# Kernel optimization log

Hardware: AMD Instinct MI355X
Metric: run time of the kernel (lower is better)

## Reference

```python
import jax, jax.numpy as jnp
import numpy as np

B, S, F, H, P, O = 512, 336, 16, 256, 48, 1

def _gru_cell(x, h, Wih, Whh, bih, bhh):
    # torch GRU gate order: r, z, n
    gx = x @ Wih.T + bih            # [B, 3H]
    gh = h @ Whh.T + bhh            # [B, 3H]
    rx, zx, nx = jnp.split(gx, 3, axis=-1)
    rh, zh, nh = jnp.split(gh, 3, axis=-1)
    r = jax.nn.sigmoid(rx + rh)
    z = jax.nn.sigmoid(zx + zh)
    n = jnp.tanh(nx + r * nh)
    return (1.0 - z) * n + z * h

def setup_inputs() -> dict:
    key = jax.random.key(0)
    ks = jax.random.split(key, 12)
    s = lambda *sh: 1.0 / np.sqrt(sh[-1])
    d = {}
    d["xb"] = jax.random.normal(ks[0], (B, S, F), dtype=jnp.float32)
    # encoder GRU (1 layer, unidirectional)
    d["enc_Wih"] = jax.random.normal(ks[1], (3 * H, F), dtype=jnp.float32) * s(F)
    d["enc_Whh"] = jax.random.normal(ks[2], (3 * H, H), dtype=jnp.float32) * s(H)
    d["enc_bih"] = jnp.zeros((3 * H,), dtype=jnp.float32)
    d["enc_bhh"] = jnp.zeros((3 * H,), dtype=jnp.float32)
    # attention linear: (H + F) -> S
    d["att_W"] = jax.random.normal(ks[3], (S, H + F), dtype=jnp.float32) * s(H + F)
    d["att_b"] = jnp.zeros((S,), dtype=jnp.float32)
    # decoder GRUCell: input H, hidden H
    d["dec_Wih"] = jax.random.normal(ks[4], (3 * H, H), dtype=jnp.float32) * s(H)
    d["dec_Whh"] = jax.random.normal(ks[5], (3 * H, H), dtype=jnp.float32) * s(H)
    d["dec_bih"] = jnp.zeros((3 * H,), dtype=jnp.float32)
    d["dec_bhh"] = jnp.zeros((3 * H,), dtype=jnp.float32)
    # decoder output: H -> F
    d["out_W"] = jax.random.normal(ks[6], (F, H), dtype=jnp.float32) * s(H)
    d["out_b"] = jnp.zeros((F,), dtype=jnp.float32)
    # final linear: F -> O
    d["lin_W"] = jax.random.normal(ks[7], (O, F), dtype=jnp.float32) * s(F)
    d["lin_b"] = jnp.zeros((O,), dtype=jnp.float32)
    return d

def reference(xb, enc_Wih, enc_Whh, enc_bih, enc_bhh, att_W, att_b,
              dec_Wih, dec_Whh, dec_bih, dec_bhh, out_W, out_b, lin_W, lin_b):
    # ---- encoder: GRU over time ----
    h0 = jnp.zeros((B, H), dtype=xb.dtype)
    xs = jnp.swapaxes(xb, 0, 1)  # [S, B, F]

    def enc_step(h, x):
        h2 = _gru_cell(x, h, enc_Wih, enc_Whh, enc_bih, enc_bhh)
        return h2, h2

    enc_hidden, enc_out = jax.lax.scan(enc_step, h0, xs)
    enc_out = jnp.swapaxes(enc_out, 0, 1)  # [B, S, H]

    # ---- decoder: per-step attention + GRUCell + output proj ----
    y0 = xb[:, -1, :]  # [B, F]

    def dec_step(carry, _):
        h, y = carry
        att_in = jnp.concatenate([h, y], axis=1)          # [B, H+F]
        attn = jax.nn.softmax(att_in @ att_W.T + att_b, axis=-1)  # [B, S]
        combine = jnp.einsum('bs,bsh->bh', attn, enc_out)  # [B, H]
        h2 = _gru_cell(combine, h, dec_Wih, dec_Whh, dec_bih, dec_bhh)
        out = h2 @ out_W.T + out_b                         # [B, F]
        return (h2, out), out

    _, outs = jax.lax.scan(dec_step, (enc_hidden, y0), None, length=P)  # [P, B, F]
    outs = jnp.swapaxes(outs, 0, 1)                        # [B, P, F]
    outs = outs @ lin_W.T + lin_b                          # [B, P, O]
    return outs.squeeze(-1)                                # [B, P]
```

## Files before the change

### kernel.cpp

```cpp
#include <hip/hip_runtime.h>
#include <cstdint>
#include <cstddef>

#define B_ 512
#define S_ 336
#define F_ 16
#define H_ 256
#define P_ 48

typedef __bf16 bhalf;
typedef __attribute__((ext_vector_type(8))) __bf16 bhalf8;
typedef __attribute__((ext_vector_type(4))) float f32x4;

#define MFMA16(A, Bv, C) __builtin_amdgcn_mfma_f32_16x16x32_bf16((A), (Bv), (C), 0, 0, 0)

__device__ __forceinline__ float fastrcp(float x) { return __builtin_amdgcn_rcpf(x); }
__device__ __forceinline__ float sigm(float x) { return fastrcp(1.0f + __expf(-x)); }
__device__ __forceinline__ float tanh_f(float x) { return 2.0f * fastrcp(1.0f + __expf(-2.0f * x)) - 1.0f; }

__device__ __forceinline__ bhalf u16_to_bf(unsigned int u) {
  return __builtin_bit_cast(__bf16, (unsigned short)u);
}
__device__ __forceinline__ unsigned short bf_to_u16(bhalf b) {
  return __builtin_bit_cast(unsigned short, b);
}

__device__ __forceinline__ bhalf8 bzero8() {
  bhalf8 v;
#pragma unroll
  for (int j = 0; j < 8; ++j) v[j] = (bhalf)0.0f;
  return v;
}

__global__ __launch_bounds__(256, 1) void enc_kernel(
    const float* __restrict__ Whh, const float* __restrict__ Wih,
    const float* __restrict__ bih, const float* __restrict__ bhh,
    const float* __restrict__ xb,
    bhalf* __restrict__ enc_out,
    float* __restrict__ hcur,
    unsigned int* __restrict__ hpack,
    unsigned int* __restrict__ flags)
{
  const int tid  = threadIdx.x;
  const int lane = tid & 63;
  const int wv   = tid >> 6;
  const int ncol = lane & 15;
  const int quad = lane >> 4;

  const int blk = blockIdx.x;
  const int g   = blk & 31;
  const int w   = blk >> 5;
  const int b0  = g * 16;
  const int i0  = w * 64 + wv * 16;

  bhalf8 bWh[3][9], bWl[3][9];
#pragma unroll
  for (int gg = 0; gg < 3; ++gg) {
    const int jrow = gg * 256 + i0 + ncol;
#pragma unroll
    for (int kt = 0; kt < 9; ++kt) {
      bhalf8 vh = bzero8(), vl = bzero8();
      if (kt < 8) {
        const float* src = Whh + (size_t)jrow * 256 + kt * 32 + quad * 8;
#pragma unroll
        for (int j = 0; j < 8; ++j) {
          const float v = src[j];
          const bhalf h = (bhalf)v;
          vh[j] = h;
          vl[j] = (bhalf)(v - (float)h);
        }
      } else if (quad < 2) {
        const float* src = Wih + (size_t)jrow * 16 + quad * 8;
#pragma unroll
        for (int j = 0; j < 8; ++j) {
          const float v = src[j];
          const bhalf h = (bhalf)v;
          vh[j] = h;
          vl[j] = (bhalf)(v - (float)h);
        }
      }
      bWh[gg][kt] = vh;
      bWl[gg][kt] = vl;
    }
  }

  const int jr = i0 + ncol;
  const float bR  = bih[jr]       + bhh[jr];
  const float bZ  = bih[256 + jr] + bhh[256 + jr];
  const float bNx = bih[512 + jr];
  const float bNh = bhh[512 + jr];

  const int bA = b0 + ncol;
  const int kA = quad * 8;

  float hold[4] = {0.0f, 0.0f, 0.0f, 0.0f};

  for (int t = 0; t < S_; ++t) {
    bhalf8 xh = bzero8(), xl = bzero8();
    if (quad < 2) {
      const float* xp = xb + ((size_t)bA * S_ + t) * F_ + quad * 8;
#pragma unroll
      for (int j = 0; j < 8; ++j) {
        const float v = __builtin_nontemporal_load(xp + j);
        const bhalf h = (bhalf)v;
        xh[j] = h;
        xl[j] = (bhalf)(v - (float)h);
      }
    }

    f32x4 aR0 = {0,0,0,0}, aR1 = {0,0,0,0}, aR2 = {0,0,0,0};
    f32x4 aZ0 = {0,0,0,0}, aZ1 = {0,0,0,0}, aZ2 = {0,0,0,0};
    f32x4 aN0 = {0,0,0,0}, aN1 = {0,0,0,0}, aN2 = {0,0,0,0};
    f32x4 aNx = {0,0,0,0};

    aR0 = MFMA16(xh, bWh[0][8], aR0);
    aR1 = MFMA16(xh, bWl[0][8], aR1);
    aR2 = MFMA16(xl, bWh[0][8], aR2);
    aZ0 = MFMA16(xh, bWh[1][8], aZ0);
    aZ1 = MFMA16(xh, bWl[1][8], aZ1);
    aZ2 = MFMA16(xl, bWh[1][8], aZ2);
    aNx = MFMA16(xh, bWh[2][8], aNx);
    aNx = MFMA16(xh, bWl[2][8], aNx);
    aNx = MFMA16(xl, bWh[2][8], aNx);

    if (t > 0) {
      const unsigned int* fp = &flags[g * 4 + (lane & 3)];
      while (__hip_atomic_load(fp, __ATOMIC_RELAXED, __HIP_MEMORY_SCOPE_AGENT) <
             (unsigned int)t)
        __builtin_amdgcn_s_sleep(1);

      const int slot = (t - 1) & 1;
      const unsigned long long* hp64 =
          (const unsigned long long*)(hpack + ((size_t)slot * B_ + bA) * H_ + kA);

      unsigned long long wbuf[32];
#pragma unroll
      for (int i = 0; i < 32; ++i)
        wbuf[i] = __hip_atomic_load(hp64 + (i >> 2) * 16 + (i & 3),
                                    __ATOMIC_RELAXED, __HIP_MEMORY_SCOPE_AGENT);

#pragma unroll
      for (int kt = 0; kt < 8; ++kt) {
        bhalf8 Ah, Al;
#pragma unroll
        for (int j2 = 0; j2 < 4; ++j2) {
          const unsigned long long w2 = wbuf[kt * 4 + j2];
          Ah[2 * j2]     = u16_to_bf((unsigned int)w2);
          Al[2 * j2]     = u16_to_bf((unsigned int)(w2 >> 16));
          Ah[2 * j2 + 1] = u16_to_bf((unsigned int)(w2 >> 32));
          Al[2 * j2 + 1] = u16_to_bf((unsigned int)(w2 >> 48));
        }
        aR0 = MFMA16(Ah, bWh[0][kt], aR0);
        aR1 = MFMA16(Ah, bWl[0][kt], aR1);
        aR2 = MFMA16(Al, bWh[0][kt], aR2);
        aZ0 = MFMA16(Ah, bWh[1][kt], aZ0);
        aZ1 = MFMA16(Ah, bWl[1][kt], aZ1);
        aZ2 = MFMA16(Al, bWh[1][kt], aZ2);
        aN0 = MFMA16(Ah, bWh[2][kt], aN0);
        aN1 = MFMA16(Ah, bWl[2][kt], aN1);
        aN2 = MFMA16(Al, bWh[2][kt], aN2);
      }
    }

    const int iL = i0 + ncol;
    bhalf his[4];
#pragma unroll
    for (int r = 0; r < 4; ++r) {
      const float sR  = aR0[r] + aR1[r] + aR2[r] + bR;
      const float sZ  = aZ0[r] + aZ1[r] + aZ2[r] + bZ;
      const float nhv = aN0[r] + aN1[r] + aN2[r] + bNh;
      const float nxv = aNx[r] + bNx;
      const float rr = sigm(sR);
      const float zz = sigm(sZ);
      const float nn = tanh_f(nxv + rr * nhv);
      const float h2 = (1.0f - zz) * nn + zz * hold[r];
      hold[r] = h2;
      his[r] = (bhalf)h2;
      const bhalf lo = (bhalf)(h2 - (float)his[r]);
      const int bb = b0 + quad * 4 + r;
      const unsigned int wrd =
          (unsigned int)bf_to_u16(his[r]) | ((unsigned int)bf_to_u16(lo) << 16);
      __hip_atomic_store(&hpack[((size_t)(t & 1) * B_ + bb) * H_ + iL], wrd,
                         __ATOMIC_RELAXED, __HIP_MEMORY_SCOPE_AGENT);
    }

    __syncthreads();
    if (tid == 0) {
      __hip_atomic_store(&flags[g * 4 + w], (unsigned int)(t + 1),
                         __ATOMIC_RELAXED, __HIP_MEMORY_SCOPE_AGENT);
    }

#pragma unroll
    for (int r = 0; r < 4; ++r) {
      const int bb = b0 + quad * 4 + r;
      __builtin_nontemporal_store(his[r], enc_out + ((size_t)bb * S_ + t) * H_ + iL);
    }
  }

#pragma unroll
  for (int r = 0; r < 4; ++r)
    hcur[(size_t)(b0 + quad * 4 + r) * H_ + i0 + ncol] = hold[r];
}

__global__ __launch_bounds__(256) void wpack_kernel(const float* __restrict__ Whh,
                                                    const float* __restrict__ Wih,
                                                    bhalf* __restrict__ wbT) {
  const int idx = blockIdx.x * 256 + threadIdx.x;
  if (idx >= 64 * 768 * 8) return;
  const int j = idx & 7;
  const int row = (idx >> 3) % 768;
  const int k8 = idx / (768 * 8);
  const int k = k8 * 8 + j;
  const float v = (k < 256) ? Whh[(size_t)row * 256 + k]
                            : Wih[(size_t)row * 256 + (k - 256)];
  wbT[idx] = (bhalf)v;
}

__global__ __launch_bounds__(256) void apack_kernel(const float* __restrict__ attW,
                                                    bhalf* __restrict__ abT) {
  const int idx = blockIdx.x * 256 + threadIdx.x;
  if (idx >= 36 * 336 * 8) return;
  const int j = idx & 7;
  const int s = (idx >> 3) % 336;
  const int k8 = idx / (8 * 336);
  const int k = k8 * 8 + j;
  abT[idx] = (k < 272) ? (bhalf)attW[(size_t)s * 272 + k] : (bhalf)0.0f;
}

__global__ __launch_bounds__(256) void dec_kernel(
    const bhalf* __restrict__ wbT,
    const bhalf* __restrict__ abT,
    const float* __restrict__ attb,
    const float* __restrict__ bih, const float* __restrict__ bhh,
    const float* __restrict__ outW, const float* __restrict__ outb,
    const float* __restrict__ linW, const float* __restrict__ linb,
    const bhalf* __restrict__ enc_out, const float* __restrict__ hcur,
    const float* __restrict__ xb, float* __restrict__ dout)
{
  __shared__ __align__(16) bhalf encL[126 * 256];
  __shared__ __align__(16) float hybuf[2][288];
  __shared__ __align__(16) float cL[256];
  __shared__ float sc[S_];
  __shared__ float pC[8][32][9];
  __shared__ float red[8];
  const int tid  = threadIdx.x;
  const int lane = tid & 63;
  const int wv   = tid >> 6;
  const int b    = blockIdx.x;
  const int jj   = tid;
  const int cg   = tid & 31;
  const int ck   = tid >> 5;
  const int s2ok = tid < 80;
  const int f_o  = tid >> 4;
  const int q_o  = tid & 15;

  {
    const bhalf8* src = (const bhalf8*)(enc_out + (size_t)b * S_ * H_);
    bhalf8* dst = (bhalf8*)encL;
    for (int it = tid; it < 126 * 32; it += 256) dst[it] = src[it];
  }

  hybuf[0][tid] = hcur[(size_t)b * H_ + tid];
  if (tid < 16) {
    hybuf[0][256 + tid] = xb[((size_t)b * S_ + (S_ - 1)) * F_ + tid];
    hybuf[1][256 + tid] = 0.0f;
  } else if (tid < 32) {
    hybuf[0][256 + tid] = 0.0f;
    hybuf[1][256 + tid] = 0.0f;
  }

  const float bRv  = bih[jj]       + bhh[jj];
  const float bZv  = bih[256 + jj] + bhh[256 + jj];
  const float bNxv = bih[512 + jj];
  const float bNhv = bhh[512 + jj];

  const float ab1 = attb[tid];
  const float ab2 = s2ok ? attb[tid + 256] : 0.0f;

  f32x4 ow[4];
  {
    const float* wrp = outW + (size_t)f_o * H_ + q_o * 16;
#pragma unroll
    for (int jv = 0; jv < 4; ++jv) ow[jv] = *(const f32x4*)(wrp + jv * 4);
  }
  const float outb_f = outb[f_o];
  const float linw_t = (tid < 16) ? linW[tid] : 0.0f;
  const float linb0  = linb[0];

  const bhalf* epC = enc_out + ((size_t)b * S_ + ck * 42) * H_ + cg * 8;
  const bhalf* epL = encL + (size_t)(ck * 42) * H_ + cg * 8;
  __syncthreads();

  for (int p = 0; p < P_; ++p) {
    float* hc = hybuf[p & 1];
    float* hn = hybuf[(p & 1) ^ 1];

    float v1, v2 = -3.0e38f;
    {
      float d0 = 0, d1 = 0, d2 = 0, d3 = 0;
#pragma unroll 4
      for (int k8 = 0; k8 < 36; ++k8) {
        const bhalf8 q = *(const bhalf8*)(abT + ((size_t)k8 * S_ + tid) * 8);
        const float* v = hc + k8 * 8;
        d0 += (float)q[0] * v[0] + (float)q[4] * v[4];
        d1 += (float)q[1] * v[1] + (float)q[5] * v[5];
        d2 += (float)q[2] * v[2] + (float)q[6] * v[6];
        d3 += (float)q[3] * v[3] + (float)q[7] * v[7];
      }
      v1 = d0 + d1 + d2 + d3 + ab1;
    }
    if (s2ok) {
      float d0 = 0, d1 = 0, d2 = 0, d3 = 0;
#pragma unroll 4
      for (int k8 = 0; k8 < 36; ++k8) {
        const bhalf8 q = *(const bhalf8*)(abT + ((size_t)k8 * S_ + tid + 256) * 8);
        const float* v = hc + k8 * 8;
        d0 += (float)q[0] * v[0] + (float)q[4] * v[4];
        d1 += (float)q[1] * v[1] + (float)q[5] * v[5];
        d2 += (float)q[2] * v[2] + (float)q[6] * v[6];
        d3 += (float)q[3] * v[3] + (float)q[7] * v[7];
      }
      v2 = d0 + d1 + d2 + d3 + ab2;
    }

    float m = fmaxf(v1, v2);
#pragma unroll
    for (int o = 32; o > 0; o >>= 1) m = fmaxf(m, __shfl_xor(m, o, 64));
    if (lane == 0) red[wv] = m;
    __syncthreads();
    const float mx = fmaxf(fmaxf(red[0], red[1]), fmaxf(red[2], red[3]));
    const float e1 = __expf(v1 - mx);
    sc[tid] = e1;
    float e2 = 0.0f;
    if (s2ok) { e2 = __expf(v2 - mx); sc[tid + 256] = e2; }
    float sum = e1 + e2;
#pragma unroll
    for (int o = 32; o > 0; o >>= 1) sum += __shfl_xor(sum, o, 64);
    if (lane == 0) red[4 + wv] = sum;
    __syncthreads();
    const float inv = fastrcp(red[4] + red[5] + red[6] + red[7]);

    {
      float a0 = 0, a1 = 0, a2 = 0, a3 = 0, a4 = 0, a5 = 0, a6 = 0, a7 = 0;
      const float* scrow = sc + ck * 42;
      if (ck < 3) {
#pragma unroll 6
        for (int s5 = 0; s5 < 42; ++s5) {
          const bhalf8 v = *(const bhalf8*)(epL + (size_t)s5 * H_);
          const float wgt = scrow[s5];
          a0 += wgt * (float)v[0];
          a1 += wgt * (float)v[1];
          a2 += wgt * (float)v[2];
          a3 += wgt * (float)v[3];
          a4 += wgt * (float)v[4];
          a5 += wgt * (float)v[5];
          a6 += wgt * (float)v[6];
          a7 += wgt * (float)v[7];
        }
      } else {
#pragma unroll 6
        for (int s5 = 0; s5 < 42; ++s5) {
          const bhalf8 v = *(const bhalf8*)(epC + (size_t)s5 * H_);
          const float wgt = scrow[s5];
          a0 += wgt * (float)v[0];
          a1 += wgt * (float)v[1];
          a2 += wgt * (float)v[2];
          a3 += wgt * (float)v[3];
          a4 += wgt * (float)v[4];
          a5 += wgt * (float)v[5];
          a6 += wgt * (float)v[6];
          a7 += wgt * (float)v[7];
        }
      }
      float* pp = pC[ck][cg];
      pp[0] = a0; pp[1] = a1; pp[2] = a2; pp[3] = a3;
      pp[4] = a4; pp[5] = a5; pp[6] = a6; pp[7] = a7;
    }
    __syncthreads();

    float r0 = 0, r1 = 0, z0 = 0, z1 = 0, nh0 = 0, nh1 = 0, nx0 = 0, nx1 = 0;
    {
      const int gg = jj >> 3, j = jj & 7;
      float ssum = 0.0f;
#pragma unroll
      for (int c = 0; c < 8; ++c) ssum += pC[c][gg][j];
      cL[jj] = ssum * inv;
    }
#pragma unroll 4
    for (int k8 = 0; k8 < 32; ++k8) {
      const bhalf* base = wbT + ((size_t)k8 * 768) * 8;
      const bhalf8 qR = *(const bhalf8*)(base + (size_t)jj * 8);
      const bhalf8 qZ = *(const bhalf8*)(base + (size_t)(256 + jj) * 8);
      const bhalf8 qN = *(const bhalf8*)(base + (size_t)(512 + jj) * 8);
      const float* v = hc + k8 * 8;
      r0 += (float)qR[0]*v[0] + (float)qR[2]*v[2] + (float)qR[4]*v[4] + (float)qR[6]*v[6];
      r1 += (float)qR[1]*v[1] + (float)qR[3]*v[3] + (float)qR[5]*v[5] + (float)qR[7]*v[7];
      z0 += (float)qZ[0]*v[0] + (float)qZ[2]*v[2] + (float)qZ[4]*v[4] + (float)qZ[6]*v[6];
      z1 += (float)qZ[1]*v[1] + (float)qZ[3]*v[3] + (float)qZ[5]*v[5] + (float)qZ[7]*v[7];
      nh0 += (float)qN[0]*v[0] + (float)qN[2]*v[2] + (float)qN[4]*v[4] + (float)qN[6]*v[6];
      nh1 += (float)qN[1]*v[1] + (float)qN[3]*v[3] + (float)qN[5]*v[5] + (float)qN[7]*v[7];
    }
    __syncthreads();
#pragma unroll 4
    for (int k8 = 32; k8 < 64; ++k8) {
      const bhalf* base = wbT + ((size_t)k8 * 768) * 8;
      const bhalf8 qR = *(const bhalf8*)(base + (size_t)jj * 8);
      const bhalf8 qZ = *(const bhalf8*)(base + (size_t)(256 + jj) * 8);
      const bhalf8 qN = *(const bhalf8*)(base + (size_t)(512 + jj) * 8);
      const float* v = cL + (k8 - 32) * 8;
      r0 += (float)qR[0]*v[0] + (float)qR[2]*v[2] + (float)qR[4]*v[4] + (float)qR[6]*v[6];
      r1 += (float)qR[1]*v[1] + (float)qR[3]*v[3] + (float)qR[5]*v[5] + (float)qR[7]*v[7];
      z0 += (float)qZ[0]*v[0] + (float)qZ[2]*v[2] + (float)qZ[4]*v[4] + (float)qZ[6]*v[6];
      z1 += (float)qZ[1]*v[1] + (float)qZ[3]*v[3] + (float)qZ[5]*v[5] + (float)qZ[7]*v[7];
      nx0 += (float)qN[0]*v[0] + (float)qN[2]*v[2] + (float)qN[4]*v[4] + (float)qN[6]*v[6];
      nx1 += (float)qN[1]*v[1] + (float)qN[3]*v[3] + (float)qN[5]*v[5] + (float)qN[7]*v[7];
    }
    {
      const float sR = r0 + r1 + bRv;
      const float sZ = z0 + z1 + bZv;
      const float nh = nh0 + nh1 + bNhv;
      const float nx = nx0 + nx1 + bNxv;
      const float rr = 1.0f / (1.0f + __expf(-sR));
      const float zz = 1.0f / (1.0f + __expf(-sZ));
      const float nn = tanhf(nx + rr * nh);
      hn[jj] = (1.0f - zz) * nn + zz * hc[jj];
    }
    __syncthreads();

    {
      const float* hv = hn + q_o * 16;
      float a0 = 0, a1 = 0, a2 = 0, a3 = 0;
#pragma unroll
      for (int jv = 0; jv < 4; ++jv) {
        const f32x4 h4 = *(const f32x4*)(hv + jv * 4);
        a0 += ow[jv][0] * h4[0]; a1 += ow[jv][1] * h4[1];
        a2 += ow[jv][2] * h4[2]; a3 += ow[jv][3] * h4[3];
      }
      float a = a0 + a1 + a2 + a3;
      a += __shfl_xor(a, 1, 64); a += __shfl_xor(a, 2, 64);
      a += __shfl_xor(a, 4, 64); a += __shfl_xor(a, 8, 64);
      if (q_o == 0) hn[256 + f_o] = a + outb_f;
    }
    __syncthreads();
    if (tid < 16) {
      float v = hn[256 + tid] * linw_t;
      v += __shfl_xor(v, 1, 64); v += __shfl_xor(v, 2, 64);
      v += __shfl_xor(v, 4, 64); v += __shfl_xor(v, 8, 64);
      if (tid == 0) dout[(size_t)b * P_ + p] = v + linb0;
    }
  }
}

extern "C" void kernel_launch(void* const* d_in, const int* in_sizes, int n_in,
                              void* d_out, int out_size, void* d_ws, size_t ws_size,
                              hipStream_t stream)
{
  (void)in_sizes; (void)n_in; (void)out_size;
  const float* xb      = (const float*)d_in[0];
  const float* enc_Wih = (const float*)d_in[1];
  const float* enc_Whh = (const float*)d_in[2];
  const float* enc_bih = (const float*)d_in[3];
  const float* enc_bhh = (const float*)d_in[4];
  const float* att_W   = (const float*)d_in[5];
  const float* att_b   = (const float*)d_in[6];
  const float* dec_Wih = (const float*)d_in[7];
  const float* dec_Whh = (const float*)d_in[8];
  const float* dec_bih = (const float*)d_in[9];
  const float* dec_bhh = (const float*)d_in[10];
  const float* out_W   = (const float*)d_in[11];
  const float* out_b   = (const float*)d_in[12];
  const float* lin_W   = (const float*)d_in[13];
  const float* lin_b   = (const float*)d_in[14];
  float* dout = (float*)d_out;

  char* ws = (char*)d_ws;
  const size_t off_enc = 0;
  const size_t off_hp  = off_enc + (size_t)B_ * S_ * H_ * 2;
  const size_t off_hc  = off_hp + (size_t)2 * B_ * H_ * 4;
  const size_t off_wb  = off_hc + (size_t)B_ * H_ * 4;
  const size_t off_ab  = off_wb + (size_t)64 * 768 * 8 * 2;
  const size_t off_fl  = off_ab + (size_t)36 * 336 * 8 * 2;
  const size_t need    = off_fl + 32 * 8 * sizeof(unsigned int);
  if (ws_size < need) return;

  bhalf* enc_out      = (bhalf*)(ws + off_enc);
  unsigned int* hpack = (unsigned int*)(ws + off_hp);
  float* hcur         = (float*)(ws + off_hc);
  bhalf* wbT          = (bhalf*)(ws + off_wb);
  bhalf* abT          = (bhalf*)(ws + off_ab);
  unsigned int* flags = (unsigned int*)(ws + off_fl);

  (void)hipMemsetAsync(flags, 0, 32 * 8 * sizeof(unsigned int), stream);
  wpack_kernel<<<(64 * 768 * 8 + 255) / 256, 256, 0, stream>>>(dec_Whh, dec_Wih, wbT);
  apack_kernel<<<(36 * 336 * 8 + 255) / 256, 256, 0, stream>>>(att_W, abT);
  enc_kernel<<<128, 256, 0, stream>>>(enc_Whh, enc_Wih, enc_bih, enc_bhh, xb,
                                      enc_out, hcur, hpack, flags);
  dec_kernel<<<B_, 256, 0, stream>>>(wbT, abT, att_b, dec_bih, dec_bhh,
                                     out_W, out_b, lin_W, lin_b,
                                     enc_out, hcur, xb, dout);
}
```

Baseline: 3.254 ms.

## Replace cross-block flag-synchronized encoder with per-block LDS recurrence

The encoder GRU previously split each 16-row batch group across 4 blocks that exchanged hidden state through global memory with atomic flags and spin-waits every timestep. It now runs one 512-thread block per batch group, keeping the hi/lo bf16 hidden state in double-buffered shared memory and synchronizing with __syncthreads. Weights are pre-packed by a new kernel into an MFMA-fragment layout and streamed from global/L2 each step rather than held in registers. This removes the inter-block spin latency, but it uses only 32 blocks and re-reads about 860 KB of weights per step, which may make each step memory-bound.

```diff
diff --git a/kernel.cpp b/kernel.cpp
--- a/kernel.cpp
+++ b/kernel.cpp
@@ -18,13 +18,6 @@
 __device__ __forceinline__ float sigm(float x) { return fastrcp(1.0f + __expf(-x)); }
 __device__ __forceinline__ float tanh_f(float x) { return 2.0f * fastrcp(1.0f + __expf(-2.0f * x)) - 1.0f; }
 
-__device__ __forceinline__ bhalf u16_to_bf(unsigned int u) {
-  return __builtin_bit_cast(__bf16, (unsigned short)u);
-}
-__device__ __forceinline__ unsigned short bf_to_u16(bhalf b) {
-  return __builtin_bit_cast(unsigned short, b);
-}
-
 __device__ __forceinline__ bhalf8 bzero8() {
   bhalf8 v;
 #pragma unroll
@@ -32,70 +25,66 @@
   return v;
 }
 
-__global__ __launch_bounds__(256, 1) void enc_kernel(
-    const float* __restrict__ Whh, const float* __restrict__ Wih,
+__global__ __launch_bounds__(256) void epack_kernel(const float* __restrict__ Whh,
+                                                    const float* __restrict__ Wih,
+                                                    bhalf* __restrict__ epk) {
+  const int idx = blockIdx.x * 256 + threadIdx.x;
+  if (idx >= 2 * 48 * 9 * 64 * 8) return;
+  const int jj   = idx & 7;
+  const int lane = (idx >> 3) & 63;
+  const int kt   = (idx >> 9) % 9;
+  const int tile = (idx / (512 * 9)) % 48;
+  const int pl   = idx / (512 * 9 * 48);
+  const int wv = tile / 6, rem = tile % 6, gg = rem >> 1, q = rem & 1;
+  const int ncol = lane & 15, quad = lane >> 4;
+  const int jrow = gg * 256 + wv * 32 + q * 16 + ncol;
+  const int k = kt * 32 + quad * 8 + jj;
+  float v = 0.0f;
+  if (k < 256) v = Whh[(size_t)jrow * 256 + k];
+  else if (k < 272) v = Wih[(size_t)jrow * 16 + (k - 256)];
+  const bhalf hi = (bhalf)v;
+  epk[idx] = (pl == 0) ? hi : (bhalf)(v - (float)hi);
+}
+
+__global__ __launch_bounds__(512, 1) void enc2_kernel(
+    const bhalf* __restrict__ epk,
     const float* __restrict__ bih, const float* __restrict__ bhh,
     const float* __restrict__ xb,
     bhalf* __restrict__ enc_out,
-    float* __restrict__ hcur,
-    unsigned int* __restrict__ hpack,
-    unsigned int* __restrict__ flags)
+    float* __restrict__ hcur)
 {
+  __shared__ __align__(16) bhalf hb[2][2][16][264];
+
   const int tid  = threadIdx.x;
   const int lane = tid & 63;
   const int wv   = tid >> 6;
   const int ncol = lane & 15;
   const int quad = lane >> 4;
-
-  const int blk = blockIdx.x;
-  const int g   = blk & 31;
-  const int w   = blk >> 5;
-  const int b0  = g * 16;
-  const int i0  = w * 64 + wv * 16;
-
-  bhalf8 bWh[3][9], bWl[3][9];
-#pragma unroll
-  for (int gg = 0; gg < 3; ++gg) {
-    const int jrow = gg * 256 + i0 + ncol;
-#pragma unroll
-    for (int kt = 0; kt < 9; ++kt) {
-      bhalf8 vh = bzero8(), vl = bzero8();
-      if (kt < 8) {
-        const float* src = Whh + (size_t)jrow * 256 + kt * 32 + quad * 8;
-#pragma unroll
-        for (int j = 0; j < 8; ++j) {
-          const float v = src[j];
-          const bhalf h = (bhalf)v;
-          vh[j] = h;
-          vl[j] = (bhalf)(v - (float)h);
-        }
-      } else if (quad < 2) {
-        const float* src = Wih + (size_t)jrow * 16 + quad * 8;
-#pragma unroll
-        for (int j = 0; j < 8; ++j) {
-          const float v = src[j];
-          const bhalf h = (bhalf)v;
-          vh[j] = h;
-          vl[j] = (bhalf)(v - (float)h);
-        }
-      }
-      bWh[gg][kt] = vh;
-      bWl[gg][kt] = vl;
-    }
-  }
-
-  const int jr = i0 + ncol;
-  const float bR  = bih[jr]       + bhh[jr];
-  const float bZ  = bih[256 + jr] + bhh[256 + jr];
-  const float bNx = bih[512 + jr];
-  const float bNh = bhh[512 + jr];
-
+  const int b0   = blockIdx.x * 16;
+  const int jb   = wv * 32;
+  const int wt   = wv * 6;
+
+  for (int i = tid; i < 2 * 16 * 264; i += 512) ((bhalf*)hb)[i] = (bhalf)0.0f;
+
+  float bRq[2], bZq[2], bNxq[2], bNhq[2];
+#pragma unroll
+  for (int q = 0; q < 2; ++q) {
+    const int jr = jb + q * 16 + ncol;
+    bRq[q]  = bih[jr]       + bhh[jr];
+    bZq[q]  = bih[256 + jr] + bhh[256 + jr];
+    bNxq[q] = bih[512 + jr];
+    bNhq[q] = bhh[512 + jr];
+  }
   const int bA = b0 + ncol;
-  const int kA = quad * 8;
-
-  float hold[4] = {0.0f, 0.0f, 0.0f, 0.0f};
+  const bhalf8* ev = (const bhalf8*)epk;
+  const f32x4 FZ = {0.0f, 0.0f, 0.0f, 0.0f};
+
+  float hold[2][4] = {{0, 0, 0, 0}, {0, 0, 0, 0}};
+  __syncthreads();
 
   for (int t = 0; t < S_; ++t) {
+    const int slot = t & 1;
+
     bhalf8 xh = bzero8(), xl = bzero8();
     if (quad < 2) {
       const float* xp = xb + ((size_t)bA * S_ + t) * F_ + quad * 8;
@@ -108,98 +97,82 @@
       }
     }
 
-    f32x4 aR0 = {0,0,0,0}, aR1 = {0,0,0,0}, aR2 = {0,0,0,0};
-    f32x4 aZ0 = {0,0,0,0}, aZ1 = {0,0,0,0}, aZ2 = {0,0,0,0};
-    f32x4 aN0 = {0,0,0,0}, aN1 = {0,0,0,0}, aN2 = {0,0,0,0};
-    f32x4 aNx = {0,0,0,0};
-
-    aR0 = MFMA16(xh, bWh[0][8], aR0);
-    aR1 = MFMA16(xh, bWl[0][8], aR1);
-    aR2 = MFMA16(xl, bWh[0][8], aR2);
-    aZ0 = MFMA16(xh, bWh[1][8], aZ0);
-    aZ1 = MFMA16(xh, bWl[1][8], aZ1);
-    aZ2 = MFMA16(xl, bWh[1][8], aZ2);
-    aNx = MFMA16(xh, bWh[2][8], aNx);
-    aNx = MFMA16(xh, bWl[2][8], aNx);
-    aNx = MFMA16(xl, bWh[2][8], aNx);
-
-    if (t > 0) {
-      const unsigned int* fp = &flags[g * 4 + (lane & 3)];
-      while (__hip_atomic_load(fp, __ATOMIC_RELAXED, __HIP_MEMORY_SCOPE_AGENT) <
-             (unsigned int)t)
-        __builtin_amdgcn_s_sleep(1);
-
-      const int slot = (t - 1) & 1;
-      const unsigned long long* hp64 =
-          (const unsigned long long*)(hpack + ((size_t)slot * B_ + bA) * H_ + kA);
-
-      unsigned long long wbuf[32];
-#pragma unroll
-      for (int i = 0; i < 32; ++i)
-        wbuf[i] = __hip_atomic_load(hp64 + (i >> 2) * 16 + (i & 3),
-                                    __ATOMIC_RELAXED, __HIP_MEMORY_SCOPE_AGENT);
-
-#pragma unroll
-      for (int kt = 0; kt < 8; ++kt) {
-        bhalf8 Ah, Al;
-#pragma unroll
-        for (int j2 = 0; j2 < 4; ++j2) {
-          const unsigned long long w2 = wbuf[kt * 4 + j2];
-          Ah[2 * j2]     = u16_to_bf((unsigned int)w2);
-          Al[2 * j2]     = u16_to_bf((unsigned int)(w2 >> 16));
-          Ah[2 * j2 + 1] = u16_to_bf((unsigned int)(w2 >> 32));
-          Al[2 * j2 + 1] = u16_to_bf((unsigned int)(w2 >> 48));
+    f32x4 a0[3][2], a1[3][2], a2[3][2], aNx[2];
+#pragma unroll
+    for (int gg = 0; gg < 3; ++gg)
+#pragma unroll
+      for (int q = 0; q < 2; ++q) { a0[gg][q] = FZ; a1[gg][q] = FZ; a2[gg][q] = FZ; }
+    aNx[0] = FZ; aNx[1] = FZ;
+
+#pragma unroll 2
+    for (int kt = 0; kt < 8; ++kt) {
+      const bhalf8 Ah = *(const bhalf8*)&hb[slot][0][ncol][kt * 32 + quad * 8];
+      const bhalf8 Al = *(const bhalf8*)&hb[slot][1][ncol][kt * 32 + quad * 8];
+#pragma unroll
+      for (int gg = 0; gg < 3; ++gg)
+#pragma unroll
+        for (int q = 0; q < 2; ++q) {
+          const int fi = ((wt + gg * 2 + q) * 9 + kt) * 64 + lane;
+          const bhalf8 Wh = ev[fi];
+          const bhalf8 Wl = ev[432 * 64 + fi];
+          a0[gg][q] = MFMA16(Ah, Wh, a0[gg][q]);
+          a1[gg][q] = MFMA16(Ah, Wl, a1[gg][q]);
+          a2[gg][q] = MFMA16(Al, Wh, a2[gg][q]);
         }
-        aR0 = MFMA16(Ah, bWh[0][kt], aR0);
-        aR1 = MFMA16(Ah, bWl[0][kt], aR1);
-        aR2 = MFMA16(Al, bWh[0][kt], aR2);
-        aZ0 = MFMA16(Ah, bWh[1][kt], aZ0);
-        aZ1 = MFMA16(Ah, bWl[1][kt], aZ1);
-        aZ2 = MFMA16(Al, bWh[1][kt], aZ2);
-        aN0 = MFMA16(Ah, bWh[2][kt], aN0);
-        aN1 = MFMA16(Ah, bWl[2][kt], aN1);
-        aN2 = MFMA16(Al, bWh[2][kt], aN2);
-      }
-    }
-
-    const int iL = i0 + ncol;
-    bhalf his[4];
-#pragma unroll
-    for (int r = 0; r < 4; ++r) {
-      const float sR  = aR0[r] + aR1[r] + aR2[r] + bR;
-      const float sZ  = aZ0[r] + aZ1[r] + aZ2[r] + bZ;
-      const float nhv = aN0[r] + aN1[r] + aN2[r] + bNh;
-      const float nxv = aNx[r] + bNx;
-      const float rr = sigm(sR);
-      const float zz = sigm(sZ);
-      const float nn = tanh_f(nxv + rr * nhv);
-      const float h2 = (1.0f - zz) * nn + zz * hold[r];
-      hold[r] = h2;
-      his[r] = (bhalf)h2;
-      const bhalf lo = (bhalf)(h2 - (float)his[r]);
-      const int bb = b0 + quad * 4 + r;
-      const unsigned int wrd =
-          (unsigned int)bf_to_u16(his[r]) | ((unsigned int)bf_to_u16(lo) << 16);
-      __hip_atomic_store(&hpack[((size_t)(t & 1) * B_ + bb) * H_ + iL], wrd,
-                         __ATOMIC_RELAXED, __HIP_MEMORY_SCOPE_AGENT);
-    }
-
-    __syncthreads();
-    if (tid == 0) {
-      __hip_atomic_store(&flags[g * 4 + w], (unsigned int)(t + 1),
-                         __ATOMIC_RELAXED, __HIP_MEMORY_SCOPE_AGENT);
-    }
-
-#pragma unroll
-    for (int r = 0; r < 4; ++r) {
-      const int bb = b0 + quad * 4 + r;
-      __builtin_nontemporal_store(his[r], enc_out + ((size_t)bb * S_ + t) * H_ + iL);
-    }
-  }
-
-#pragma unroll
-  for (int r = 0; r < 4; ++r)
-    hcur[(size_t)(b0 + quad * 4 + r) * H_ + i0 + ncol] = hold[r];
+    }
+#pragma unroll
+    for (int gg = 0; gg < 2; ++gg)
+#pragma unroll
+      for (int q = 0; q < 2; ++q) {
+        const int fi = ((wt + gg * 2 + q) * 9 + 8) * 64 + lane;
+        const bhalf8 Wh = ev[fi];
+        const bhalf8 Wl = ev[432 * 64 + fi];
+        a0[gg][q] = MFMA16(xh, Wh, a0[gg][q]);
+        a1[gg][q] = MFMA16(xh, Wl, a1[gg][q]);
+        a2[gg][q] = MFMA16(xl, Wh, a2[gg][q]);
+      }
+#pragma unroll
+    for (int q = 0; q < 2; ++q) {
+      const int fi = ((wt + 4 + q) * 9 + 8) * 64 + lane;
+      const bhalf8 Wh = ev[fi];
+      const bhalf8 Wl = ev[432 * 64 + fi];
+      aNx[q] = MFMA16(xh, Wh, aNx[q]);
+      aNx[q] = MFMA16(xh, Wl, aNx[q]);
+      aNx[q] = MFMA16(xl, Wh, aNx[q]);
+    }
+
+#pragma unroll
+    for (int q = 0; q < 2; ++q) {
+      const int j = jb + q * 16 + ncol;
+#pragma unroll
+      for (int r = 0; r < 4; ++r) {
+        const float sR  = a0[0][q][r] + a1[0][q][r] + a2[0][q][r] + bRq[q];
+        const float sZ  = a0[1][q][r] + a1[1][q][r] + a2[1][q][r] + bZq[q];
+        const float nhv = a0[2][q][r] + a1[2][q][r] + a2[2][q][r] + bNhq[q];
+        const float nxv = aNx[q][r] + bNxq[q];
+        const float rr = sigm(sR);
+        const float zz = sigm(sZ);
+        const float nn = tanh_f(nxv + rr * nhv);
+        const float h2 = (1.0f - zz) * nn + zz * hold[q][r];
+        hold[q][r] = h2;
+        const bhalf hi = (bhalf)h2;
+        const bhalf lo = (bhalf)(h2 - (float)hi);
+        const int bl = quad * 4 + r;
+        hb[slot ^ 1][0][bl][j] = hi;
+        hb[slot ^ 1][1][bl][j] = lo;
+        __builtin_nontemporal_store(hi, enc_out + ((size_t)(b0 + bl) * S_ + t) * H_ + j);
+      }
+    }
+    __syncthreads();
+  }
+
+#pragma unroll
+  for (int q = 0; q < 2; ++q) {
+    const int j = jb + q * 16 + ncol;
+#pragma unroll
+    for (int r = 0; r < 4; ++r)
+      hcur[(size_t)(b0 + quad * 4 + r) * H_ + j] = hold[q][r];
+  }
 }
 
 __global__ __launch_bounds__(256) void wpack_kernel(const float* __restrict__ Whh,
@@ -475,26 +448,23 @@
 
   char* ws = (char*)d_ws;
   const size_t off_enc = 0;
-  const size_t off_hp  = off_enc + (size_t)B_ * S_ * H_ * 2;
-  const size_t off_hc  = off_hp + (size_t)2 * B_ * H_ * 4;
+  const size_t off_hc  = off_enc + (size_t)B_ * S_ * H_ * 2;
   const size_t off_wb  = off_hc + (size_t)B_ * H_ * 4;
   const size_t off_ab  = off_wb + (size_t)64 * 768 * 8 * 2;
-  const size_t off_fl  = off_ab + (size_t)36 * 336 * 8 * 2;
-  const size_t need    = off_fl + 32 * 8 * sizeof(unsigned int);
+  const size_t off_ep  = off_ab + (size_t)36 * 336 * 8 * 2;
+  const size_t need    = off_ep + (size_t)2 * 48 * 9 * 64 * 8 * 2;
   if (ws_size < need) return;
 
-  bhalf* enc_out      = (bhalf*)(ws + off_enc);
-  unsigned int* hpack = (unsigned int*)(ws + off_hp);
-  float* hcur         = (float*)(ws + off_hc);
-  bhalf* wbT          = (bhalf*)(ws + off_wb);
-  bhalf* abT          = (bhalf*)(ws + off_ab);
-  unsigned int* flags = (unsigned int*)(ws + off_fl);
-
-  (void)hipMemsetAsync(flags, 0, 32 * 8 * sizeof(unsigned int), stream);
+  bhalf* enc_out = (bhalf*)(ws + off_enc);
+  float* hcur    = (float*)(ws + off_hc);
+  bhalf* wbT     = (bhalf*)(ws + off_wb);
+  bhalf* abT     = (bhalf*)(ws + off_ab);
+  bhalf* epk     = (bhalf*)(ws + off_ep);
+
   wpack_kernel<<<(64 * 768 * 8 + 255) / 256, 256, 0, stream>>>(dec_Whh, dec_Wih, wbT);
   apack_kernel<<<(36 * 336 * 8 + 255) / 256, 256, 0, stream>>>(att_W, abT);
-  enc_kernel<<<128, 256, 0, stream>>>(enc_Whh, enc_Wih, enc_bih, enc_bhh, xb,
-                                      enc_out, hcur, hpack, flags);
+  epack_kernel<<<(2 * 48 * 9 * 64 * 8 + 255) / 256, 256, 0, stream>>>(enc_Whh, enc_Wih, epk);
+  enc2_kernel<<<32, 512, 0, stream>>>(epk, enc_bih, enc_bhh, xb, enc_out, hcur);
   dec_kernel<<<B_, 256, 0, stream>>>(wbT, abT, att_b, dec_bih, dec_bhh,
                                      out_W, out_b, lin_W, lin_b,
                                      enc_out, hcur, xb, dout);
```

New measurement: 5.469 ms. 1.68x slower.
